# Optimization experiments

Measured on AMD Instinct MI355X. Metric: run time of the kernel, lower is better.

Reference implementation:

```python
import jax, jax.numpy as jnp
import numpy as np

DIM = 4096
N_HEADS = 32
N_KV_HEADS = 8
HEAD_DIM = DIM // N_HEADS  # 128
SEQLEN = 2048
BATCH = 2
ROPE_THETA = 10000.0


def _precompute_freqs(seqlen, head_dim, theta):
    # matches torchtitan precompute_freqs_cis: freqs over even indices
    freqs = 1.0 / (theta ** (np.arange(0, head_dim, 2)[: head_dim // 2].astype(np.float32) / head_dim))
    t = np.arange(seqlen, dtype=np.float32)
    ang = np.outer(t, freqs)  # (S, head_dim//2)
    return jnp.asarray(np.cos(ang)), jnp.asarray(np.sin(ang))


def setup_inputs() -> dict:
    key = jax.random.key(0)
    kx, kq, kk, kv, ko = jax.random.split(key, 5)
    x = jax.random.normal(kx, (BATCH, SEQLEN, DIM), dtype=jnp.float32)
    wq = jax.random.normal(kq, (N_HEADS * HEAD_DIM, DIM), dtype=jnp.float32) * 0.02
    wk = jax.random.normal(kk, (N_KV_HEADS * HEAD_DIM, DIM), dtype=jnp.float32) * 0.02
    wv = jax.random.normal(kv, (N_KV_HEADS * HEAD_DIM, DIM), dtype=jnp.float32) * 0.02
    wo = jax.random.normal(ko, (DIM, N_HEADS * HEAD_DIM), dtype=jnp.float32) * 0.02
    cos, sin = _precompute_freqs(SEQLEN, HEAD_DIM, ROPE_THETA)
    return {"x": x, "cos": cos, "sin": sin, "wq": wq, "wk": wk, "wv": wv, "wo": wo}


def _apply_rope(t, cos, sin):
    # t: (B, S, H, hd); pairs (t[...,2i], t[...,2i+1]) rotated by angle
    tr = t.reshape(*t.shape[:-1], -1, 2)
    a, b = tr[..., 0], tr[..., 1]
    c = cos[None, :, None, :]  # (1, S, 1, hd//2)
    s = sin[None, :, None, :]
    out = jnp.stack([a * c - b * s, a * s + b * c], axis=-1)
    return out.reshape(t.shape)


def reference(x, cos, sin, wq, wk, wv, wo):
    B, S, D = x.shape
    hd = 2 * cos.shape[-1]
    H = wq.shape[0] // hd
    KVH = wk.shape[0] // hd
    n_rep = H // KVH

    q = (x @ wq.T).reshape(B, S, H, hd)
    k = (x @ wk.T).reshape(B, S, KVH, hd)
    v = (x @ wv.T).reshape(B, S, KVH, hd)

    q = _apply_rope(q, cos, sin)
    k = _apply_rope(k, cos, sin)

    # GQA: repeat_interleave kv heads (kept implicit via reshape of q into groups)
    qg = q.reshape(B, S, KVH, n_rep, hd)
    scale = 1.0 / jnp.sqrt(jnp.asarray(hd, dtype=x.dtype))
    # scores: (B, KVH, n_rep, S_q, S_k)
    scores = jnp.einsum("bsgrd,btgd->bgrst", qg, k) * scale
    causal = jnp.tril(jnp.ones((S, S), dtype=bool))
    scores = jnp.where(causal[None, None, None], scores, jnp.asarray(-1e30, dtype=scores.dtype))
    probs = jax.nn.softmax(scores, axis=-1)
    out = jnp.einsum("bgrst,btgd->bsgrd", probs, v).reshape(B, S, H * hd)
    return out @ wo.T
```

## Files before the change

### kernel.cpp

```cpp
#include <hip/hip_runtime.h>
#include <hip/hip_bf16.h>
#include <stdint.h>

#define DIM    4096
#define NH     32
#define NKVH   8
#define HD     128
#define SEQ    2048
#define BATCH  2
#define MTOT   (BATCH*SEQ)
#define SCALE  0.08838834764831845f

typedef __bf16 bf16_t;
typedef __bf16 bf16x8 __attribute__((ext_vector_type(8)));
typedef float  f32x4  __attribute__((ext_vector_type(4)));

#define AS1 __attribute__((address_space(1)))
#define AS3 __attribute__((address_space(3)))

__device__ __forceinline__ void gload_lds16(const void* g, void* l) {
    __builtin_amdgcn_global_load_lds((const AS1 void*)g, (AS3 void*)l, 16, 0, 0);
}

__device__ __forceinline__ void fence_barrier() {
    asm volatile("" ::: "memory");
    __builtin_amdgcn_s_barrier();
    asm volatile("" ::: "memory");
}

__global__ __launch_bounds__(256)
void cvt_f32_bf16(const float* __restrict__ in, bf16_t* __restrict__ out, int n4) {
    for (int i = blockIdx.x * blockDim.x + threadIdx.x; i < n4;
         i += gridDim.x * blockDim.x) {
        float4 v = reinterpret_cast<const float4*>(in)[i];
        union { bf16_t b[4]; uint2 u; } t;
        t.b[0] = (bf16_t)v.x; t.b[1] = (bf16_t)v.y;
        t.b[2] = (bf16_t)v.z; t.b[3] = (bf16_t)v.w;
        reinterpret_cast<uint2*>(out)[i] = t.u;
    }
}

__global__ __launch_bounds__(256)
void cvt_weights(const float* __restrict__ wq, const float* __restrict__ wk,
                 const float* __restrict__ wv, const float* __restrict__ wo,
                 bf16_t* __restrict__ out) {
    const int n0 = DIM * DIM / 4;
    const int n1 = NKVH * HD * DIM / 4;
    const int n2 = NKVH * HD * DIM / 4;
    const int n3 = DIM * DIM / 4;
    const int ntot = n0 + n1 + n2 + n3;
    for (int i = blockIdx.x * blockDim.x + threadIdx.x; i < ntot;
         i += gridDim.x * blockDim.x) {
        const float* src;
        int k = i;
        if (k < n0) src = wq;
        else if ((k -= n0) < n1) src = wk;
        else if ((k -= n1) < n2) src = wv;
        else { k -= n2; src = wo; }
        float4 v = reinterpret_cast<const float4*>(src)[k];
        union { bf16_t b[4]; uint2 u; } t;
        t.b[0] = (bf16_t)v.x; t.b[1] = (bf16_t)v.y;
        t.b[2] = (bf16_t)v.z; t.b[3] = (bf16_t)v.w;
        reinterpret_cast<uint2*>(out)[i] = t.u;
    }
}


__device__ __forceinline__ void stage_half(const bf16_t* gbase, int kt, int h,
                                           bf16_t* ldsdst, int tid, int w) {
#pragma unroll
    for (int t2 = 0; t2 < 2; ++t2) {
        int s = t2 * 512 + tid;
        int r = s >> 3, c = s & 7;
        gload_lds16(gbase + (size_t)(h * 128 + r) * DIM + kt + ((c ^ (r & 7)) * 8),
                    ldsdst + (size_t)(t2 * 512 + w * 64) * 8);
    }
}

__device__ __forceinline__ void read_a8(bf16x8* a, const bf16_t* Ahalf,
                                        int kk, int lr, int lg) {
#pragma unroll
    for (int mi = 0; mi < 8; ++mi) {
        int r = mi * 16 + lr;
        a[mi] = *(const bf16x8*)(Ahalf + r * 64 + ((kk * 4 + lg) ^ (r & 7)) * 8);
    }
}

__device__ __forceinline__ void read_b4(bf16x8* b, const bf16_t* Bhalf,
                                        int kk, int rb, int lg) {
#pragma unroll
    for (int ni = 0; ni < 4; ++ni) {
        int r = rb + ni * 16;
        b[ni] = *(const bf16x8*)(Bhalf + r * 64 + ((kk * 4 + lg) ^ (r & 7)) * 8);
    }
}

template<int MODE>
__global__ __launch_bounds__(512, 2)
void gemm8(const bf16_t* __restrict__ A,
           const bf16_t* __restrict__ B0,
           const bf16_t* __restrict__ B1,
           float* __restrict__ outF,
           bf16_t* __restrict__ outQ,
           bf16_t* __restrict__ outV,
           const float* __restrict__ cosT,
           const float* __restrict__ sinT) {
    __shared__ __align__(16) bf16_t As[2][2][128 * 64];
    __shared__ __align__(16) bf16_t Bs[2][2][128 * 64];

    const int tid = threadIdx.x;
    const int l = tid & 63;
    const int w = tid >> 6;
    const int wm = w >> 2, wn = w & 3;
    const int lr = l & 15, lg = l >> 4;
    const int rb = (wn & 1) * 64 + lr;
    const int bh2 = wn >> 1;

    const int rowBase = blockIdx.x * 256;
    const int ct = blockIdx.y;

    const bf16_t* Ap = A + (size_t)rowBase * DIM;
    const bf16_t* Bp;
    if (MODE == 2) Bp = (ct < 4) ? (B0 + (size_t)ct * 256 * DIM)
                                 : (B1 + (size_t)(ct - 4) * 256 * DIM);
    else           Bp = B0 + (size_t)ct * 256 * DIM;

    f32x4 acc[8][4] = {};
    bf16x8 a0[8], a1[8], b0[4], b1[4];

    const int NT = DIM / 64;

    stage_half(Ap, 0,  0, &As[0][0][0], tid, w);
    stage_half(Ap, 0,  1, &As[0][1][0], tid, w);
    stage_half(Bp, 0,  0, &Bs[0][0][0], tid, w);
    stage_half(Bp, 0,  1, &Bs[0][1][0], tid, w);
    stage_half(Ap, 64, 0, &As[1][0][0], tid, w);
    stage_half(Ap, 64, 1, &As[1][1][0], tid, w);
    stage_half(Bp, 64, 0, &Bs[1][0][0], tid, w);
    stage_half(Bp, 64, 1, &Bs[1][1][0], tid, w);
    asm volatile("s_waitcnt vmcnt(8)" ::: "memory");
    fence_barrier();
    read_a8(a0, &As[0][wm][0], 0, lr, lg);
    read_b4(b0, &Bs[0][bh2][0], 0, rb, lg);

    for (int j = 0; j < NT; ++j) {
        const int buf = j & 1;

        read_a8(a1, &As[buf][wm][0], 1, lr, lg);
        read_b4(b1, &Bs[buf][bh2][0], 1, rb, lg);
        __builtin_amdgcn_s_setprio(1);
#pragma unroll
        for (int mi = 0; mi < 8; ++mi) {
            acc[mi][0] = __builtin_amdgcn_mfma_f32_16x16x32_bf16(a0[mi], b0[0], acc[mi][0], 0, 0, 0);
            acc[mi][1] = __builtin_amdgcn_mfma_f32_16x16x32_bf16(a0[mi], b0[1], acc[mi][1], 0, 0, 0);
            acc[mi][2] = __builtin_amdgcn_mfma_f32_16x16x32_bf16(a0[mi], b0[2], acc[mi][2], 0, 0, 0);
            acc[mi][3] = __builtin_amdgcn_mfma_f32_16x16x32_bf16(a0[mi], b0[3], acc[mi][3], 0, 0, 0);
        }
        __builtin_amdgcn_s_setprio(0);
        asm volatile("s_waitcnt lgkmcnt(0)" ::: "memory");
        fence_barrier();

        {
            const int t2i = (j + 2 < NT) ? (j + 2) : (NT - 1);
            const int kt2 = t2i * 64;
            bf16_t* Adst0 = &As[t2i & 1][0][0];
            bf16_t* Bdst0 = &Bs[t2i & 1][0][0];
            stage_half(Ap, kt2, 0, Adst0, tid, w);
            stage_half(Ap, kt2, 1, Adst0 + 128 * 64, tid, w);
            stage_half(Bp, kt2, 0, Bdst0, tid, w);
            stage_half(Bp, kt2, 1, Bdst0 + 128 * 64, tid, w);
        }
        __builtin_amdgcn_s_setprio(1);
#pragma unroll
        for (int mi = 0; mi < 8; ++mi) {
            acc[mi][0] = __builtin_amdgcn_mfma_f32_16x16x32_bf16(a1[mi], b1[0], acc[mi][0], 0, 0, 0);
            acc[mi][1] = __builtin_amdgcn_mfma_f32_16x16x32_bf16(a1[mi], b1[1], acc[mi][1], 0, 0, 0);
            acc[mi][2] = __builtin_amdgcn_mfma_f32_16x16x32_bf16(a1[mi], b1[2], acc[mi][2], 0, 0, 0);
            acc[mi][3] = __builtin_amdgcn_mfma_f32_16x16x32_bf16(a1[mi], b1[3], acc[mi][3], 0, 0, 0);
        }
        __builtin_amdgcn_s_setprio(0);
        asm volatile("s_waitcnt vmcnt(8)" ::: "memory");
        fence_barrier();
        if (j + 1 < NT) {
            read_a8(a0, &As[buf ^ 1][wm][0], 0, lr, lg);
            read_b4(b0, &Bs[buf ^ 1][bh2][0], 0, rb, lg);
        }
    }

#pragma unroll
    for (int mi = 0; mi < 8; ++mi) {
        int gmBase = rowBase + wm * 128 + mi * 16 + lg * 4;
#pragma unroll
        for (int ni = 0; ni < 4; ++ni) {
            f32x4 v4 = acc[mi][ni];
            int gn = ct * 256 + wn * 64 + ni * 16 + lr;
            if (MODE == 0) {
#pragma unroll
                for (int i = 0; i < 4; ++i)
                    outF[(size_t)(gmBase + i) * DIM + gn] = v4[i];
            } else if (MODE == 1) {
                int h = gn >> 7, d = gn & 127, pi2 = d >> 1;
#pragma unroll
                for (int i = 0; i < 4; ++i) {
                    float v = v4[i];
                    float pvv = __shfl_xor(v, 1);
                    int gm = gmBase + i;
                    int bb = gm >> 11, sidx = gm & (SEQ - 1);
                    float c = cosT[sidx * 64 + pi2], sn = sinT[sidx * 64 + pi2];
                    float o = (d & 1) ? (pvv * sn + v * c) : (v * c - pvv * sn);
                    outQ[((size_t)(bb * NH + h) * SEQ + sidx) * HD + d] = (bf16_t)o;
                }
            } else {
                if (ct < 4) {
                    int h = gn >> 7, d = gn & 127, pi2 = d >> 1;
#pragma unroll
                    for (int i = 0; i < 4; ++i) {
                        float v = v4[i];
                        float pvv = __shfl_xor(v, 1);
                        int gm = gmBase + i;
                        int bb = gm >> 11, sidx = gm & (SEQ - 1);
                        float c = cosT[sidx * 64 + pi2], sn = sinT[sidx * 64 + pi2];
                        float o = (d & 1) ? (pvv * sn + v * c) : (v * c - pvv * sn);
                        outQ[((size_t)(bb * NKVH + h) * SEQ + sidx) * HD + d] = (bf16_t)o;
                    }
                } else {
                    int gnv = (ct - 4) * 256 + wn * 64 + ni * 16 + lr;
                    int kvh = gnv >> 7, d = gnv & 127;
#pragma unroll
                    for (int i = 0; i < 4; ++i) {
                        float dummy = __shfl_xor(v4[i], 1); (void)dummy;
                        int gm = gmBase + i;
                        int bb = gm >> 11, sidx = gm & (SEQ - 1);
                        outV[((size_t)(bb * NKVH + kvh) * HD + d) * SEQ + sidx] = (bf16_t)v4[i];
                    }
                }
            }
        }
    }
}

__global__ __launch_bounds__(256, 2)
void attn_fwd(const bf16_t* __restrict__ Qr,
              const bf16_t* __restrict__ Kr,
              const bf16_t* __restrict__ Vt,
              bf16_t* __restrict__ Ob) {
    __shared__ __align__(16) bf16_t Ks[2][64 * 128];
    __shared__ __align__(16) bf16_t Vs[2][128 * 64];
    __shared__ __align__(16) bf16_t Ps[4][32 * 64];

    const int tid = threadIdx.x;
    const int l  = tid & 63;
    const int w  = tid >> 6;
    const int lr = l & 15, lg = l >> 4;
    const int e  = lr & 7;

    const int qt  = 15 - (blockIdx.x >> 6);
    const int bh  = blockIdx.x & 63;
    const int b   = bh >> 5;
    const int h   = bh & 31;
    const int kvh = h >> 2;
    const int q0  = qt * 128;
    const int nt  = 2 * qt + 2;
    const int qmin = q0 + w * 32;

    const bf16_t* kbase = Kr + (size_t)(b * NKVH + kvh) * SEQ * HD;
    const bf16_t* vbase = Vt + (size_t)(b * NKVH + kvh) * HD * SEQ;

    bf16x8 qf[2][4];
    const bf16_t* qp = Qr + ((size_t)(b * NH + h) * SEQ + qmin + lr) * HD;
#pragma unroll
    for (int mi = 0; mi < 2; ++mi)
#pragma unroll
        for (int kk = 0; kk < 4; ++kk)
            qf[mi][kk] = *(const bf16x8*)(qp + (size_t)mi * 16 * HD + kk * 32 + lg * 8);

    f32x4 oacc[2][8] = {};
    float mrow[2] = {-1e30f, -1e30f};
    float lsum[2] = {0.f, 0.f};

#pragma unroll
    for (int t2 = 0; t2 < 4; ++t2) {
        int s = t2 * 256 + tid;
        { int r = s >> 4, g = (s & 15) ^ (r & 7);
          gload_lds16(kbase + (size_t)r * HD + g * 8,
                      &Ks[0][(size_t)(t2 * 256 + w * 64) * 8]); }
        { int r = s >> 3, g = (s & 7) ^ (r & 7);
          gload_lds16(vbase + (size_t)r * SEQ + g * 8,
                      &Vs[0][(size_t)(t2 * 256 + w * 64) * 8]); }
    }
    __syncthreads();

    int cur = 0;
    for (int t = 0; t < nt; ++t) {
        if (t + 1 < nt) {
            const int kv1 = (t + 1) * 64;
#pragma unroll
            for (int t2 = 0; t2 < 4; ++t2) {
                int s = t2 * 256 + tid;
                { int r = s >> 4, g = (s & 15) ^ (r & 7);
                  gload_lds16(kbase + (size_t)(kv1 + r) * HD + g * 8,
                              &Ks[cur ^ 1][(size_t)(t2 * 256 + w * 64) * 8]); }
                { int r = s >> 3, g = (s & 7) ^ (r & 7);
                  gload_lds16(vbase + (size_t)r * SEQ + kv1 + g * 8,
                              &Vs[cur ^ 1][(size_t)(t2 * 256 + w * 64) * 8]); }
            }
        }

        const bool active = (t * 64) <= (qmin + 31);
        if (active) {
            const bool needMask = (t * 64 + 63) > qmin;

            f32x4 sf[2][4] = {};
#pragma unroll
            for (int kk = 0; kk < 4; ++kk)
#pragma unroll
                for (int nf = 0; nf < 4; ++nf) {
                    bf16x8 kf = *(const bf16x8*)(
                        &Ks[cur][(nf * 16 + lr) * 128 + ((kk * 4 + lg) ^ e) * 8]);
#pragma unroll
                    for (int mi = 0; mi < 2; ++mi)
                        sf[mi][nf] = __builtin_amdgcn_mfma_f32_16x16x32_bf16(
                            kf, qf[mi][kk], sf[mi][nf], 0, 0, 0);
                }

            float aO[2][4];
#pragma unroll
            for (int mi = 0; mi < 2; ++mi) {
                const int qrow = qmin + mi * 16 + lr;
                float mt = -1e30f;
#pragma unroll
                for (int nf = 0; nf < 4; ++nf)
#pragma unroll
                    for (int i = 0; i < 4; ++i) {
                        float sc = sf[mi][nf][i] * SCALE;
                        if (needMask && (t * 64 + nf * 16 + lg * 4 + i) > qrow)
                            sc = -1e30f;
                        sf[mi][nf][i] = sc;
                        mt = fmaxf(mt, sc);
                    }
                mt = fmaxf(mt, __shfl_xor(mt, 16));
                mt = fmaxf(mt, __shfl_xor(mt, 32));
                float mnew = fmaxf(mrow[mi], mt);
                float alpha = __expf(mrow[mi] - mnew);
                mrow[mi] = mnew;
                float rs = 0.f;
#pragma unroll
                for (int nf = 0; nf < 4; ++nf)
#pragma unroll
                    for (int i = 0; i < 4; ++i) {
                        float p = __expf(sf[mi][nf][i] - mnew);
                        sf[mi][nf][i] = p;
                        rs += p;
                    }
                rs += __shfl_xor(rs, 16);
                rs += __shfl_xor(rs, 32);
                lsum[mi] = lsum[mi] * alpha + rs;
#pragma unroll
                for (int i = 0; i < 4; ++i)
                    aO[mi][i] = __shfl(alpha, lg * 4 + i);
            }

#pragma unroll
            for (int mi = 0; mi < 2; ++mi)
#pragma unroll
                for (int df = 0; df < 8; ++df)
#pragma unroll
                    for (int i = 0; i < 4; ++i)
                        oacc[mi][df][i] *= aO[mi][i];

#pragma unroll
            for (int mi = 0; mi < 2; ++mi)
#pragma unroll
                for (int nf = 0; nf < 4; ++nf) {
                    union { bf16_t bb[4]; uint2 u; } pk;
#pragma unroll
                    for (int i = 0; i < 4; ++i) pk.bb[i] = (bf16_t)sf[mi][nf][i];
                    int addr = (mi * 16 + lr) * 64 +
                               (((nf * 2 + (lg >> 1)) ^ e) << 3) + (lg & 1) * 4;
                    *(uint2*)(&Ps[w][addr]) = pk.u;
                }
            asm volatile("s_waitcnt lgkmcnt(0)" ::: "memory");
            __builtin_amdgcn_sched_barrier(0);

            bf16x8 pf[2][2];
#pragma unroll
            for (int mi = 0; mi < 2; ++mi)
#pragma unroll
                for (int k2 = 0; k2 < 2; ++k2)
                    pf[mi][k2] = *(const bf16x8*)(
                        &Ps[w][(mi * 16 + lr) * 64 + ((k2 * 4 + lg) ^ e) * 8]);
#pragma unroll
            for (int df = 0; df < 8; ++df)
#pragma unroll
                for (int k2 = 0; k2 < 2; ++k2) {
                    bf16x8 vf = *(const bf16x8*)(
                        &Vs[cur][(df * 16 + lr) * 64 + ((k2 * 4 + lg) ^ e) * 8]);
#pragma unroll
                    for (int mi = 0; mi < 2; ++mi)
                        oacc[mi][df] = __builtin_amdgcn_mfma_f32_16x16x32_bf16(
                            pf[mi][k2], vf, oacc[mi][df], 0, 0, 0);
                }
        }
        __syncthreads();
        cur ^= 1;
    }

#pragma unroll
    for (int mi = 0; mi < 2; ++mi) {
        float ls[4];
#pragma unroll
        for (int i = 0; i < 4; ++i)
            ls[i] = 1.f / __shfl(lsum[mi], lg * 4 + i);
#pragma unroll
        for (int df = 0; df < 8; ++df)
#pragma unroll
            for (int i = 0; i < 4; ++i) {
                float o = oacc[mi][df][i] * ls[i];
                int gm = b * SEQ + qmin + mi * 16 + lg * 4 + i;
                int gn = h * HD + df * 16 + lr;
                Ob[(size_t)gm * DIM + gn] = (bf16_t)o;
            }
    }
}

extern "C" void kernel_launch(void* const* d_in, const int* in_sizes, int n_in,
                              void* d_out, int out_size, void* d_ws, size_t ws_size,
                              hipStream_t stream) {
    const float* x    = (const float*)d_in[0];
    const float* cosT = (const float*)d_in[1];
    const float* sinT = (const float*)d_in[2];
    const float* wq   = (const float*)d_in[3];
    const float* wk   = (const float*)d_in[4];
    const float* wv   = (const float*)d_in[5];
    const float* wo   = (const float*)d_in[6];

    bf16_t* p = (bf16_t*)d_ws;
    bf16_t* xb  = p; p += (size_t)MTOT * DIM;
    bf16_t* wqb = p; p += (size_t)DIM * DIM;
    bf16_t* wkb = p; p += (size_t)NKVH * HD * DIM;
    bf16_t* wvb = p; p += (size_t)NKVH * HD * DIM;
    bf16_t* wob = p; p += (size_t)DIM * DIM;
    bf16_t* Qr  = p; p += (size_t)MTOT * DIM;
    bf16_t* Kr  = p; p += (size_t)BATCH * NKVH * SEQ * HD;
    bf16_t* Vt  = p; p += (size_t)BATCH * NKVH * HD * SEQ;
    bf16_t* Ob  = p; p += (size_t)MTOT * DIM;

    cvt_f32_bf16<<<2048, 256, 0, stream>>>(x, xb, MTOT * DIM / 4);
    cvt_weights<<<2048, 256, 0, stream>>>(wq, wk, wv, wo, wqb);

    gemm8<1><<<dim3(16, 16), 512, 0, stream>>>(
        xb, wqb, nullptr, nullptr, Qr, nullptr, cosT, sinT);
    gemm8<2><<<dim3(16, 8), 512, 0, stream>>>(
        xb, wkb, wvb, nullptr, Kr, Vt, cosT, sinT);

    attn_fwd<<<1024, 256, 0, stream>>>(Qr, Kr, Vt, Ob);

    gemm8<0><<<dim3(16, 16), 512, 0, stream>>>(
        Ob, wob, nullptr, (float*)d_out, nullptr, nullptr, nullptr, nullptr);
}
```

Measured before the change: 520.1 us.

## Fuse Q/K/V projections into one GEMM launch and interleave LDS staging with MFMA

Treats the converted wq/wk/wv weights as one contiguous matrix so that a single 16x24 grid GEMM computes Q, K and V together. The epilogue picks the RoPE-Q, RoPE-K or transposed-V store based on the column tile. This removes a kernel launch and the tail imbalance of the small K/V grid. The main loop is also split into quarter-steps that interleave the A and B LDS reads and global-to-LDS staging with half of the MFMAs, adding extra barriers. This relies on cvt_weights laying out wq, wk, wv and wo contiguously.

```diff
diff --git a/kernel.cpp b/kernel.cpp
--- a/kernel.cpp
+++ b/kernel.cpp
@@ -99,9 +99,9 @@
 __global__ __launch_bounds__(512, 2)
 void gemm8(const bf16_t* __restrict__ A,
            const bf16_t* __restrict__ B0,
-           const bf16_t* __restrict__ B1,
            float* __restrict__ outF,
            bf16_t* __restrict__ outQ,
+           bf16_t* __restrict__ outK,
            bf16_t* __restrict__ outV,
            const float* __restrict__ cosT,
            const float* __restrict__ sinT) {
@@ -120,10 +120,7 @@
     const int ct = blockIdx.y;
 
     const bf16_t* Ap = A + (size_t)rowBase * DIM;
-    const bf16_t* Bp;
-    if (MODE == 2) Bp = (ct < 4) ? (B0 + (size_t)ct * 256 * DIM)
-                                 : (B1 + (size_t)(ct - 4) * 256 * DIM);
-    else           Bp = B0 + (size_t)ct * 256 * DIM;
+    const bf16_t* Bp = B0 + (size_t)ct * 256 * DIM;
 
     f32x4 acc[8][4] = {};
     bf16x8 a0[8], a1[8], b0[4], b1[4];
@@ -145,40 +142,58 @@
 
     for (int j = 0; j < NT; ++j) {
         const int buf = j & 1;
-
-        read_a8(a1, &As[buf][wm][0], 1, lr, lg);
-        read_b4(b1, &Bs[buf][bh2][0], 1, rb, lg);
+        const bf16_t* Ahalf = &As[buf][wm][0];
+        const bf16_t* Bhalf = &Bs[buf][bh2][0];
+        const int t2i = (j + 2 < NT) ? (j + 2) : (NT - 1);
+        const int kt2 = t2i * 64;
+        bf16_t* Adst = &As[t2i & 1][0][0];
+        bf16_t* Bdst = &Bs[t2i & 1][0][0];
+
+        read_a8(a1, Ahalf, 1, lr, lg);
         __builtin_amdgcn_s_setprio(1);
 #pragma unroll
         for (int mi = 0; mi < 8; ++mi) {
             acc[mi][0] = __builtin_amdgcn_mfma_f32_16x16x32_bf16(a0[mi], b0[0], acc[mi][0], 0, 0, 0);
             acc[mi][1] = __builtin_amdgcn_mfma_f32_16x16x32_bf16(a0[mi], b0[1], acc[mi][1], 0, 0, 0);
+        }
+        __builtin_amdgcn_s_setprio(0);
+        __builtin_amdgcn_sched_barrier(0);
+        fence_barrier();
+
+        read_b4(b1, Bhalf, 1, rb, lg);
+        __builtin_amdgcn_s_setprio(1);
+#pragma unroll
+        for (int mi = 0; mi < 8; ++mi) {
             acc[mi][2] = __builtin_amdgcn_mfma_f32_16x16x32_bf16(a0[mi], b0[2], acc[mi][2], 0, 0, 0);
             acc[mi][3] = __builtin_amdgcn_mfma_f32_16x16x32_bf16(a0[mi], b0[3], acc[mi][3], 0, 0, 0);
         }
         __builtin_amdgcn_s_setprio(0);
+        __builtin_amdgcn_sched_barrier(0);
         asm volatile("s_waitcnt lgkmcnt(0)" ::: "memory");
         fence_barrier();
 
-        {
-            const int t2i = (j + 2 < NT) ? (j + 2) : (NT - 1);
-            const int kt2 = t2i * 64;
-            bf16_t* Adst0 = &As[t2i & 1][0][0];
-            bf16_t* Bdst0 = &Bs[t2i & 1][0][0];
-            stage_half(Ap, kt2, 0, Adst0, tid, w);
-            stage_half(Ap, kt2, 1, Adst0 + 128 * 64, tid, w);
-            stage_half(Bp, kt2, 0, Bdst0, tid, w);
-            stage_half(Bp, kt2, 1, Bdst0 + 128 * 64, tid, w);
-        }
+        stage_half(Ap, kt2, 0, Adst, tid, w);
+        stage_half(Ap, kt2, 1, Adst + 128 * 64, tid, w);
         __builtin_amdgcn_s_setprio(1);
 #pragma unroll
         for (int mi = 0; mi < 8; ++mi) {
             acc[mi][0] = __builtin_amdgcn_mfma_f32_16x16x32_bf16(a1[mi], b1[0], acc[mi][0], 0, 0, 0);
             acc[mi][1] = __builtin_amdgcn_mfma_f32_16x16x32_bf16(a1[mi], b1[1], acc[mi][1], 0, 0, 0);
+        }
+        __builtin_amdgcn_s_setprio(0);
+        __builtin_amdgcn_sched_barrier(0);
+        fence_barrier();
+
+        stage_half(Bp, kt2, 0, Bdst, tid, w);
+        stage_half(Bp, kt2, 1, Bdst + 128 * 64, tid, w);
+        __builtin_amdgcn_s_setprio(1);
+#pragma unroll
+        for (int mi = 0; mi < 8; ++mi) {
             acc[mi][2] = __builtin_amdgcn_mfma_f32_16x16x32_bf16(a1[mi], b1[2], acc[mi][2], 0, 0, 0);
             acc[mi][3] = __builtin_amdgcn_mfma_f32_16x16x32_bf16(a1[mi], b1[3], acc[mi][3], 0, 0, 0);
         }
         __builtin_amdgcn_s_setprio(0);
+        __builtin_amdgcn_sched_barrier(0);
         asm volatile("s_waitcnt vmcnt(8)" ::: "memory");
         fence_barrier();
         if (j + 1 < NT) {
@@ -198,20 +213,8 @@
 #pragma unroll
                 for (int i = 0; i < 4; ++i)
                     outF[(size_t)(gmBase + i) * DIM + gn] = v4[i];
-            } else if (MODE == 1) {
-                int h = gn >> 7, d = gn & 127, pi2 = d >> 1;
-#pragma unroll
-                for (int i = 0; i < 4; ++i) {
-                    float v = v4[i];
-                    float pvv = __shfl_xor(v, 1);
-                    int gm = gmBase + i;
-                    int bb = gm >> 11, sidx = gm & (SEQ - 1);
-                    float c = cosT[sidx * 64 + pi2], sn = sinT[sidx * 64 + pi2];
-                    float o = (d & 1) ? (pvv * sn + v * c) : (v * c - pvv * sn);
-                    outQ[((size_t)(bb * NH + h) * SEQ + sidx) * HD + d] = (bf16_t)o;
-                }
             } else {
-                if (ct < 4) {
+                if (ct < 16) {
                     int h = gn >> 7, d = gn & 127, pi2 = d >> 1;
 #pragma unroll
                     for (int i = 0; i < 4; ++i) {
@@ -221,11 +224,24 @@
                         int bb = gm >> 11, sidx = gm & (SEQ - 1);
                         float c = cosT[sidx * 64 + pi2], sn = sinT[sidx * 64 + pi2];
                         float o = (d & 1) ? (pvv * sn + v * c) : (v * c - pvv * sn);
-                        outQ[((size_t)(bb * NKVH + h) * SEQ + sidx) * HD + d] = (bf16_t)o;
+                        outQ[((size_t)(bb * NH + h) * SEQ + sidx) * HD + d] = (bf16_t)o;
+                    }
+                } else if (ct < 20) {
+                    int kn = gn - 4096;
+                    int h = kn >> 7, d = kn & 127, pi2 = d >> 1;
+#pragma unroll
+                    for (int i = 0; i < 4; ++i) {
+                        float v = v4[i];
+                        float pvv = __shfl_xor(v, 1);
+                        int gm = gmBase + i;
+                        int bb = gm >> 11, sidx = gm & (SEQ - 1);
+                        float c = cosT[sidx * 64 + pi2], sn = sinT[sidx * 64 + pi2];
+                        float o = (d & 1) ? (pvv * sn + v * c) : (v * c - pvv * sn);
+                        outK[((size_t)(bb * NKVH + h) * SEQ + sidx) * HD + d] = (bf16_t)o;
                     }
                 } else {
-                    int gnv = (ct - 4) * 256 + wn * 64 + ni * 16 + lr;
-                    int kvh = gnv >> 7, d = gnv & 127;
+                    int vn = gn - 5120;
+                    int kvh = vn >> 7, d = vn & 127;
 #pragma unroll
                     for (int i = 0; i < 4; ++i) {
                         float dummy = __shfl_xor(v4[i], 1); (void)dummy;
@@ -436,25 +452,22 @@
 
     bf16_t* p = (bf16_t*)d_ws;
     bf16_t* xb  = p; p += (size_t)MTOT * DIM;
-    bf16_t* wqb = p; p += (size_t)DIM * DIM;
-    bf16_t* wkb = p; p += (size_t)NKVH * HD * DIM;
-    bf16_t* wvb = p; p += (size_t)NKVH * HD * DIM;
-    bf16_t* wob = p; p += (size_t)DIM * DIM;
+    bf16_t* wb  = p; p += (size_t)(DIM + 2 * NKVH * HD + DIM) * DIM;
     bf16_t* Qr  = p; p += (size_t)MTOT * DIM;
     bf16_t* Kr  = p; p += (size_t)BATCH * NKVH * SEQ * HD;
     bf16_t* Vt  = p; p += (size_t)BATCH * NKVH * HD * SEQ;
     bf16_t* Ob  = p; p += (size_t)MTOT * DIM;
 
+    bf16_t* wob = wb + (size_t)(DIM + 2 * NKVH * HD) * DIM;
+
     cvt_f32_bf16<<<2048, 256, 0, stream>>>(x, xb, MTOT * DIM / 4);
-    cvt_weights<<<2048, 256, 0, stream>>>(wq, wk, wv, wo, wqb);
-
-    gemm8<1><<<dim3(16, 16), 512, 0, stream>>>(
-        xb, wqb, nullptr, nullptr, Qr, nullptr, cosT, sinT);
-    gemm8<2><<<dim3(16, 8), 512, 0, stream>>>(
-        xb, wkb, wvb, nullptr, Kr, Vt, cosT, sinT);
+    cvt_weights<<<2048, 256, 0, stream>>>(wq, wk, wv, wo, wb);
+
+    gemm8<3><<<dim3(16, 24), 512, 0, stream>>>(
+        xb, wb, nullptr, Qr, Kr, Vt, cosT, sinT);
 
     attn_fwd<<<1024, 256, 0, stream>>>(Qr, Kr, Vt, Ob);
 
     gemm8<0><<<dim3(16, 16), 512, 0, stream>>>(
-        Ob, wob, nullptr, (float*)d_out, nullptr, nullptr, nullptr, nullptr);
-}
+        Ob, wob, (float*)d_out, nullptr, nullptr, nullptr, nullptr, nullptr);
+}
```

Measured after the change: 526.2 us. No clear change (+1.2%).
